# Kernel tuning notes

Hardware: AMD Instinct MI355X
Metric: run time of the kernel (lower is better)

Reference implementation:

```python
import jax, jax.numpy as jnp
import numpy as np

H, DH, M, ITERS, DIM = 8, 64, 256, 6, 512
SCALE = DH ** -0.5


def setup_inputs() -> dict:
    key = jax.random.key(0)
    ks = jax.random.split(key, 6)
    b, n, nz = 4, 8192, 4096  # multiples of M=256 -> padding branch is a no-op
    s = DIM ** -0.5
    x = jax.random.normal(ks[0], (b, n, DIM), jnp.float32)
    z = jax.random.normal(ks[1], (b, nz, DIM), jnp.float32)
    W_q = jax.random.normal(ks[2], (DIM, H * DH), jnp.float32) * s      # to_qkv[0] (no bias)
    W_kv = jax.random.normal(ks[3], (DIM, 2 * H * DH), jnp.float32) * s  # to_qkv[1] (no bias)
    W_out = jax.random.normal(ks[4], (H * DH, DIM), jnp.float32) * s     # to_out Linear
    b_out = jax.random.normal(ks[5], (DIM,), jnp.float32) * 0.01
    return {"x": x, "z": z, "W_q": W_q, "W_kv": W_kv, "W_out": W_out, "b_out": b_out}


def moore_penrose_pinv(a, iters=ITERS):
    # Newton-Schulz iterative pseudo-inverse (faithful to moore_penrose_iter_pinv)
    abs_a = jnp.abs(a)
    col = abs_a.sum(axis=-1)
    row = abs_a.sum(axis=-2)
    zt = jnp.swapaxes(a, -1, -2) / (jnp.max(col) * jnp.max(row))
    I = jnp.eye(a.shape[-1], dtype=a.dtype)
    for _ in range(iters):
        az = a @ zt
        zt = 0.25 * zt @ (13.0 * I - az @ (15.0 * I - az @ (7.0 * I - az)))
    return zt


def reference(x, z, W_q, W_kv, W_out, b_out):
    b, n, _ = x.shape
    nz = z.shape[1]
    l, lz = n // M, nz // M  # landmark group sizes (n, nz are multiples of M)

    # projections (dropout=0.1 is inactive at inference; self.norm is never applied in forward)
    q = (x @ W_q).reshape(b, n, H, DH).transpose(0, 2, 1, 3) * SCALE   # [b,h,n,dh]
    kv = z @ W_kv
    k = kv[..., : H * DH].reshape(b, nz, H, DH).transpose(0, 2, 1, 3)  # [b,h,nz,dh]
    v = kv[..., H * DH :].reshape(b, nz, H, DH).transpose(0, 2, 1, 3)  # [b,h,nz,dh]

    # landmarks: mean over groups of l (resp. lz) consecutive tokens
    q_land = q.reshape(b, H, M, l, DH).sum(axis=3) / l    # [b,h,M,dh]
    k_land = k.reshape(b, H, M, lz, DH).sum(axis=3) / lz  # [b,h,M,dh]

    sim1 = jnp.einsum('bhid,bhjd->bhij', q, k_land)       # [b,h,n,M]
    sim2 = jnp.einsum('bhid,bhjd->bhij', q_land, k_land)  # [b,h,M,M]
    sim3 = jnp.einsum('bhid,bhjd->bhij', q_land, k)       # [b,h,M,nz]
    attn1 = jax.nn.softmax(sim1, axis=-1)
    attn2 = jax.nn.softmax(sim2, axis=-1)
    attn3 = jax.nn.softmax(sim3, axis=-1)

    attn2_inv = moore_penrose_pinv(attn2)
    # (attn1 @ attn2_inv) @ (attn3 @ v) computed small-first for efficiency; same math
    out = attn1 @ (attn2_inv @ (attn3 @ v))               # [b,h,n,dh]  (residual=False)

    out = out.transpose(0, 2, 1, 3).reshape(b, n, H * DH)
    out = out @ W_out + b_out
    return x + out
```

## Files before the change

kernel.cpp:

```cpp
#include <hip/hip_runtime.h>

typedef unsigned short u16;
typedef __attribute__((ext_vector_type(8))) short bf16x8s;
typedef __attribute__((ext_vector_type(4))) float f32x4;

#define DEV static __device__ __forceinline__

DEV float b2f(u16 v) { return __uint_as_float(((unsigned)v) << 16); }
DEV u16 f2b(float f) {
  unsigned r;
  asm("v_cvt_pk_bf16_f32 %0, %1, %1" : "=v"(r) : "v"(f));
  return (u16)r;
}
DEV unsigned f2b2(float a, float b) {
  unsigned r;
  asm("v_cvt_pk_bf16_f32 %0, %1, %2" : "=v"(r) : "v"(a), "v"(b));
  return r;
}

#define GLL(gp, lp)                                                            \
  __builtin_amdgcn_global_load_lds(                                            \
      (const __attribute__((address_space(1))) unsigned int*)(gp),             \
      (__attribute__((address_space(3))) unsigned int*)(lp), 16, 0, 0)

#define MFMA __builtin_amdgcn_mfma_f32_16x16x32_bf16

__global__ __launch_bounds__(256) void k_f2bxz(const float* __restrict__ x,
                                               const float* __restrict__ z,
                                               u16* __restrict__ xb,
                                               u16* __restrict__ zb) {
  long i = (long)blockIdx.x * 256 + threadIdx.x;
  const float* src;
  u16* dst;
  long j;
  if (i < 4194304) { src = x; dst = xb; j = i; }
  else { src = z; dst = zb; j = i - 4194304; }
  float4 v = *(const float4*)(src + j * 4);
  unsigned* d = (unsigned*)(dst + j * 4);
  d[0] = f2b2(v.x, v.y);
  d[1] = f2b2(v.z, v.w);
}

__global__ __launch_bounds__(256) void k_wt3(const float* __restrict__ Wq,
                                             const float* __restrict__ Wkv,
                                             const float* __restrict__ Wo,
                                             u16* __restrict__ wqt,
                                             u16* __restrict__ wkvt,
                                             u16* __restrict__ wot) {
  int e = blockIdx.x * 256 + threadIdx.x;
  const float* W;
  u16* Wt;
  int N, le;
  if (e < 262144) { W = Wq; Wt = wqt; N = 512; le = e; }
  else if (e < 786432) { W = Wkv; Wt = wkvt; N = 1024; le = e - 262144; }
  else { W = Wo; Wt = wot; N = 512; le = e - 786432; }
  int nn = le >> 9, kk = le & 511;
  Wt[le] = f2b(W[(long)kk * N + nn]);
}

template <int MODE>
__global__ __launch_bounds__(256, 2) void k_gemm128(
    const u16* __restrict__ A, const u16* __restrict__ Bm, void* __restrict__ C0,
    void* __restrict__ C1, const float* __restrict__ xres,
    const float* __restrict__ bias, int K) {
  const int nwg = gridDim.x * gridDim.y;
  const int orig = blockIdx.y * gridDim.x + blockIdx.x;
  const int qq = nwg >> 3, rr = nwg & 7;
  const int xcd = orig & 7, loc = orig >> 3;
  const int swz = (xcd < rr ? xcd * (qq + 1) : rr * (qq + 1) + (xcd - rr) * qq) + loc;
  const int m0 = (swz / gridDim.x) << 7, n0 = (swz % gridDim.x) << 7;
  const int t = threadIdx.x, lane = t & 63, w = t >> 6;
  const int wm = (w >> 1) << 6, wn = (w & 1) << 6;
  const int fr = lane & 15, g = lane >> 4;
  __shared__ u16 As[8192];
  __shared__ u16 Bs[8192];
  f32x4 acc[4][4] = {};
  const int srow = t >> 3, scs = t & 7;
  for (int k0 = 0; k0 < K; k0 += 64) {
    __syncthreads();
#pragma unroll
    for (int i = 0; i < 4; ++i) {
      int row = srow + (i << 5), cs = scs;
      GLL(A + (long)(m0 + row) * K + k0 + ((cs ^ (row & 7)) << 3),
          &As[(i << 11) + (w << 9)]);
      GLL(Bm + (long)(n0 + row) * K + k0 + ((cs ^ (row & 7)) << 3),
          &Bs[(i << 11) + (w << 9)]);
    }
    __syncthreads();
#pragma unroll
    for (int ks = 0; ks < 2; ++ks) {
      bf16x8s af[4], bf[4];
#pragma unroll
      for (int fi = 0; fi < 4; ++fi) {
        int row = wm + fi * 16 + fr;
        af[fi] = *(const bf16x8s*)((const char*)As + row * 128 +
                                   (((ks * 4 + g) ^ (row & 7)) << 4));
      }
#pragma unroll
      for (int fj = 0; fj < 4; ++fj) {
        int row = wn + fj * 16 + fr;
        bf[fj] = *(const bf16x8s*)((const char*)Bs + row * 128 +
                                   (((ks * 4 + g) ^ (row & 7)) << 4));
      }
#pragma unroll
      for (int fi = 0; fi < 4; ++fi)
#pragma unroll
        for (int fj = 0; fj < 4; ++fj)
          acc[fi][fj] = MFMA(af[fi], bf[fj], acc[fi][fj], 0, 0, 0);
    }
  }
  const int crow = g << 2;
#pragma unroll
  for (int fi = 0; fi < 4; ++fi)
#pragma unroll
    for (int fj = 0; fj < 4; ++fj)
#pragma unroll
      for (int r = 0; r < 4; ++r) {
        int row = m0 + wm + fi * 16 + crow + r;
        int col = n0 + wn + fj * 16 + fr;
        float v = acc[fi][fj][r];
        if (MODE == 0) {
          int b = row >> 13, n = row & 8191, h = col >> 6, dh = col & 63;
          ((u16*)C0)[((((long)(b * 8 + h)) << 13) + n) * 64 + dh] = f2b(v * 0.125f);
        } else if (MODE == 1) {
          int b = row >> 12, nz = row & 4095;
          if (col < 512) {
            int h = col >> 6, dh = col & 63;
            ((u16*)C0)[((((long)(b * 8 + h)) << 12) + nz) * 64 + dh] = f2b(v);
          } else {
            int c2 = col - 512, h = c2 >> 6, dh = c2 & 63;
            ((u16*)C1)[((((long)(b * 8 + h) * 64 + dh)) << 12) + nz] = f2b(v);
          }
        } else if (MODE == 2) {
          long idx = ((long)row << 9) + col;
          ((float*)C0)[idx] = v + xres[idx] + bias[col];
        }
      }
}

__global__ __launch_bounds__(256) void k_land2(const u16* __restrict__ qb,
                                               const u16* __restrict__ kb,
                                               u16* __restrict__ qlh,
                                               u16* __restrict__ qll,
                                               u16* __restrict__ klh,
                                               u16* __restrict__ kll) {
  int pidx = blockIdx.x * 4 + (threadIdx.x >> 6);
  const u16* src;
  u16 *hi, *lo;
  int ntok, l;
  float inv;
  if (pidx < 8192) { src = qb; hi = qlh; lo = qll; ntok = 8192; l = 32; inv = 1.f / 32.f; }
  else { src = kb; hi = klh; lo = kll; ntok = 4096; l = 16; inv = 1.f / 16.f; pidx -= 8192; }
  int d = threadIdx.x & 63;
  int bh = pidx >> 8, m = pidx & 255;
  const u16* s = src + ((long)bh * ntok + (long)m * l) * 64 + d;
  float sum = 0.f;
  for (int j = 0; j < l; ++j) sum += b2f(s[j * 64]);
  sum *= inv;
  long o = ((long)bh * 256 + m) * 64 + d;
  u16 h = f2b(sum);
  hi[o] = h;
  lo[o] = f2b(sum - b2f(h));
}

__global__ __launch_bounds__(256, 2) void k_sim2(
    const u16* __restrict__ qlh, const u16* __restrict__ qll,
    const u16* __restrict__ klh, const u16* __restrict__ kll,
    float* __restrict__ attn2, u16* __restrict__ aNhi, u16* __restrict__ aNlo) {
  const int rb = blockIdx.x, bh = blockIdx.y;
  const int t = threadIdx.x, lane = t & 63, w = t >> 6;
  const int fr = lane & 15, g = lane >> 4;
  __shared__ char lds[65536];
  {
    const u16* kh = klh + (long)bh * 16384;
    const u16* kl = kll + (long)bh * 16384;
    int srow8 = lane >> 3, cs7 = lane & 7;
#pragma unroll
    for (int i = 0; i < 8; ++i) {
      int slab = w * 8 + i;
      int krow = slab * 8 + srow8;
      GLL(kh + krow * 64 + ((cs7 ^ (krow & 7)) << 3), lds + slab * 1024);
      GLL(kl + krow * 64 + ((cs7 ^ (krow & 7)) << 3), lds + 32768 + slab * 1024);
    }
  }
  long qoff = ((long)bh * 256 + rb * 64 + w * 16 + fr) * 64;
  bf16x8s qh0 = *(const bf16x8s*)(qlh + qoff + g * 8);
  bf16x8s qh1 = *(const bf16x8s*)(qlh + qoff + 32 + g * 8);
  bf16x8s ql0 = *(const bf16x8s*)(qll + qoff + g * 8);
  bf16x8s ql1 = *(const bf16x8s*)(qll + qoff + 32 + g * 8);
  __syncthreads();
  f32x4 s[16];
#pragma unroll
  for (int c = 0; c < 16; ++c) {
    int j = (c << 4) + fr;
    int o0 = j * 128 + ((g ^ (j & 7)) << 4);
    int o1 = j * 128 + (((4 + g) ^ (j & 7)) << 4);
    bf16x8s kh0 = *(const bf16x8s*)(lds + o0);
    bf16x8s kh1 = *(const bf16x8s*)(lds + o1);
    bf16x8s kl0 = *(const bf16x8s*)(lds + 32768 + o0);
    bf16x8s kl1 = *(const bf16x8s*)(lds + 32768 + o1);
    f32x4 zz = {};
    zz = MFMA(qh0, kh0, zz, 0, 0, 0);
    zz = MFMA(qh1, kh1, zz, 0, 0, 0);
    zz = MFMA(qh0, kl0, zz, 0, 0, 0);
    zz = MFMA(qh1, kl1, zz, 0, 0, 0);
    zz = MFMA(ql0, kh0, zz, 0, 0, 0);
    zz = MFMA(ql1, kh1, zz, 0, 0, 0);
    s[c] = zz;
  }
  float li[4];
#pragma unroll
  for (int r = 0; r < 4; ++r) {
    float m = s[0][r];
#pragma unroll
    for (int c = 1; c < 16; ++c) m = fmaxf(m, s[c][r]);
    m = fmaxf(m, __shfl_xor(m, 1, 64));
    m = fmaxf(m, __shfl_xor(m, 2, 64));
    m = fmaxf(m, __shfl_xor(m, 4, 64));
    m = fmaxf(m, __shfl_xor(m, 8, 64));
    float l = 0.f;
#pragma unroll
    for (int c = 0; c < 16; ++c) {
      float e = __expf(s[c][r] - m);
      s[c][r] = e;
      l += e;
    }
    l += __shfl_xor(l, 1, 64);
    l += __shfl_xor(l, 2, 64);
    l += __shfl_xor(l, 4, 64);
    l += __shfl_xor(l, 8, 64);
    li[r] = 1.f / l;
  }
#pragma unroll
  for (int c = 0; c < 16; ++c)
#pragma unroll
    for (int r = 0; r < 4; ++r) {
      int row = rb * 64 + w * 16 + (g << 2) + r;
      int col = (c << 4) + fr;
      long idx = ((long)bh << 16) + ((long)row << 8) + col;
      float p = s[c][r] * li[r];
      attn2[idx] = p;
      u16 h = f2b(p);
      aNhi[idx] = h;
      aNlo[idx] = f2b(p - b2f(h));
    }
}

__global__ __launch_bounds__(256) void k_colmax(const float* __restrict__ attn2,
                                                unsigned* __restrict__ cmax) {
  int bh = blockIdx.x, j = threadIdx.x, lane = j & 63, w = j >> 6;
  const float* p = attn2 + ((long)bh << 16) + j;
  float s = 0.f;
  for (int m = 0; m < 256; ++m) s += p[m * 256];
  float mx = s;
  for (int o = 1; o < 64; o <<= 1) mx = fmaxf(mx, __shfl_xor(mx, o, 64));
  __shared__ float r1[4];
  if (lane == 0) r1[w] = mx;
  __syncthreads();
  if (j == 0) {
    mx = fmaxf(fmaxf(r1[0], r1[1]), fmaxf(r1[2], r1[3]));
    atomicMax(cmax, __float_as_uint(mx));
  }
}

__global__ __launch_bounds__(256, 2) void k_t1part(
    const u16* __restrict__ qlb, const u16* __restrict__ kb,
    const u16* __restrict__ vtb, float* __restrict__ opart,
    float* __restrict__ pm_, float* __restrict__ pl_) {
  int orig = blockIdx.x;
  int xcd = orig & 7, idx = orig >> 3;
  int p = xcd * 16 + (idx >> 2);
  int rb = idx & 3;
  int bh = p >> 2, kc = p & 3;
  const int t = threadIdx.x, lane = t & 63, w = t >> 6;
  const int fr = lane & 15, g = lane >> 4;
  __shared__ char lds[65536];
  const u16* qrow = qlb + ((long)bh * 256 + rb * 64 + w * 16 + fr) * 64;
  bf16x8s qa0 = *(const bf16x8s*)(qrow + g * 8);
  bf16x8s qa1 = *(const bf16x8s*)(qrow + 32 + g * 8);
  f32x4 o[4] = {};
  float m[4] = {-3e38f, -3e38f, -3e38f, -3e38f};
  float l[4] = {};
  const long kbase = (long)bh * 262144;
  for (int cc = 0; cc < 4; ++cc) {
    int c0 = kc * 1024 + cc * 256;
    __syncthreads();
#pragma unroll
    for (int i = 0; i < 8; ++i) {
      int seg = (i << 8) + t, row = seg >> 3, cs = seg & 7;
      GLL(kb + kbase + (long)(c0 + row) * 64 + ((cs ^ (row & 7)) << 3),
          lds + (i << 12) + (w << 10));
    }
#pragma unroll
    for (int i = 0; i < 8; ++i) {
      int seg = (i << 8) + t, row = seg >> 5, cs = seg & 31;
      GLL(vtb + kbase + (long)row * 4096 + c0 + ((cs ^ (row & 7)) << 3),
          lds + 32768 + (i << 12) + (w << 10));
    }
    __syncthreads();
    f32x4 s[16];
#pragma unroll
    for (int c = 0; c < 16; ++c) {
      int j = c * 16 + fr;
      bf16x8s b0 = *(const bf16x8s*)(lds + j * 128 + ((g ^ (j & 7)) << 4));
      bf16x8s b1 = *(const bf16x8s*)(lds + j * 128 + (((4 + g) ^ (j & 7)) << 4));
      f32x4 zz = {};
      zz = MFMA(qa0, b0, zz, 0, 0, 0);
      zz = MFMA(qa1, b1, zz, 0, 0, 0);
      s[c] = zz;
    }
    float sc[4];
#pragma unroll
    for (int r = 0; r < 4; ++r) {
      float pm = s[0][r];
#pragma unroll
      for (int c = 1; c < 16; ++c) pm = fmaxf(pm, s[c][r]);
      pm = fmaxf(pm, __shfl_xor(pm, 1, 64));
      pm = fmaxf(pm, __shfl_xor(pm, 2, 64));
      pm = fmaxf(pm, __shfl_xor(pm, 4, 64));
      pm = fmaxf(pm, __shfl_xor(pm, 8, 64));
      float mn = fmaxf(m[r], pm);
      sc[r] = __expf(m[r] - mn);
      m[r] = mn;
    }
#pragma unroll
    for (int r = 0; r < 4; ++r) {
      float su = 0.f;
#pragma unroll
      for (int c = 0; c < 16; ++c) {
        float e = __expf(s[c][r] - m[r]);
        s[c][r] = e;
        su += e;
      }
      su += __shfl_xor(su, 1, 64);
      su += __shfl_xor(su, 2, 64);
      su += __shfl_xor(su, 4, 64);
      su += __shfl_xor(su, 8, 64);
      l[r] = l[r] * sc[r] + su;
    }
#pragma unroll
    for (int d = 0; d < 4; ++d)
#pragma unroll
      for (int r = 0; r < 4; ++r) o[d][r] *= sc[r];
    __syncthreads();
#pragma unroll
    for (int c = 0; c < 16; ++c)
#pragma unroll
      for (int r = 0; r < 4; ++r) {
        int row = (w << 4) + (g << 2) + r;
        int byin = (c << 5) + (fr << 1);
        *(u16*)(lds + row * 512 + (byin ^ ((row & 7) << 4))) = f2b(s[c][r]);
      }
    asm volatile("s_waitcnt lgkmcnt(0)" ::: "memory");
    __builtin_amdgcn_sched_barrier(0);
#pragma unroll
    for (int ss = 0; ss < 8; ++ss) {
      int prow = (w << 4) + fr;
      bf16x8s ap = *(const bf16x8s*)(lds + prow * 512 +
                                     (((ss * 64) + (g << 4)) ^ ((prow & 7) << 4)));
#pragma unroll
      for (int d = 0; d < 4; ++d) {
        int dh = (d << 4) + fr;
        bf16x8s bv = *(const bf16x8s*)(lds + 32768 + dh * 512 +
                                       (((ss * 4 + g) ^ (dh & 7)) << 4));
        o[d] = MFMA(ap, bv, o[d], 0, 0, 0);
      }
    }
  }
  __syncthreads();
  float* lf = (float*)lds;
#pragma unroll
  for (int d = 0; d < 4; ++d)
#pragma unroll
    for (int r = 0; r < 4; ++r)
      lf[((w << 4) + (g << 2) + r) * 76 + (d << 4) + fr] = o[d][r];
  __syncthreads();
  const long pb = (long)(bh * 4 + kc) * 256 + rb * 64;
#pragma unroll
  for (int i = 0; i < 4; ++i) {
    int row = i * 16 + (t >> 4);
    int c4 = (t & 15) << 2;
    float4 v = *(const float4*)&lf[row * 76 + c4];
    *(float4*)&opart[(pb + row) * 64 + c4] = v;
  }
  if (fr == 0) {
#pragma unroll
    for (int r = 0; r < 4; ++r) {
      int lr = (w << 4) + (g << 2) + r;
      pm_[pb + lr] = m[r];
      pl_[pb + lr] = l[r];
    }
  }
}

__global__ __launch_bounds__(256) void k_t1merge(
    const float* __restrict__ opart, const float* __restrict__ pm_,
    const float* __restrict__ pl_, u16* __restrict__ T1thi,
    u16* __restrict__ T1tlo) {
  const int rb = blockIdx.x, bh = blockIdx.y;
  const int t = threadIdx.x;
#pragma unroll
  for (int rp = 0; rp < 4; ++rp) {
    int row = rb * 64 + rp * 16 + (t >> 4);
    int dh4 = (t & 15) << 2;
    float pmv[4], M = -3e38f;
#pragma unroll
    for (int i = 0; i < 4; ++i) {
      pmv[i] = pm_[(long)(bh * 4 + i) * 256 + row];
      M = fmaxf(M, pmv[i]);
    }
    float L = 0.f, wt[4];
#pragma unroll
    for (int i = 0; i < 4; ++i) {
      wt[i] = __expf(pmv[i] - M);
      L += pl_[(long)(bh * 4 + i) * 256 + row] * wt[i];
    }
    float4 acc = {0.f, 0.f, 0.f, 0.f};
#pragma unroll
    for (int i = 0; i < 4; ++i) {
      float4 v = *(const float4*)&opart[((long)(bh * 4 + i) * 256 + row) * 64 + dh4];
      acc.x += v.x * wt[i]; acc.y += v.y * wt[i];
      acc.z += v.z * wt[i]; acc.w += v.w * wt[i];
    }
    float invL = 1.f / L;
    float vv[4] = {acc.x * invL, acc.y * invL, acc.z * invL, acc.w * invL};
#pragma unroll
    for (int e = 0; e < 4; ++e) {
      int dh = dh4 + e;
      long idx = (long)bh * 16384 + (long)dh * 256 + row;
      u16 h = f2b(vv[e]);
      T1thi[idx] = h;
      T1tlo[idx] = f2b(vv[e] - b2f(h));
    }
  }
}

template <int NP>
__global__ __launch_bounds__(256) void k_nn_mfma(
    const u16* __restrict__ Ahi, const u16* __restrict__ Alo,
    const u16* __restrict__ Bthi, const u16* __restrict__ Btlo,
    u16* __restrict__ CNhi, u16* __restrict__ CNlo,
    u16* __restrict__ CThi, u16* __restrict__ CTlo,
    int Nc, float sab, float sa, float cdiag) {
  const int bz = blockIdx.z;
  const long offA = (long)bz << 16;
  const long offB = (long)bz * ((long)Nc << 8);
  const int m0 = blockIdx.y << 6, n0 = blockIdx.x << 6;
  const int t = threadIdx.x, lane = t & 63, w = t >> 6;
  const int wm = (w >> 1) << 5, wn = (w & 1) << 5;
  const int fr = lane & 15, g = lane >> 4;
  __shared__ u16 lds[16384];
  u16* LAh = lds;
  u16* LAl = lds + 4096;
  u16* LBh = lds + 8192;
  u16* LBl = lds + 12288;
  f32x4 acc[2][2] = {};
  const int srow8 = lane >> 3, cs = lane & 7;
  for (int k0 = 0; k0 < 256; k0 += 64) {
    __syncthreads();
#pragma unroll
    for (int j = 0; j < 2; ++j) {
      int slab = w * 2 + j;
      int row = slab * 8 + srow8;
      long asrc = offA + (long)(m0 + row) * 256 + k0 + ((cs ^ (row & 7)) << 3);
      long bsrc = offB + (long)(n0 + row) * 256 + k0 + ((cs ^ (row & 7)) << 3);
      GLL(Ahi + asrc, LAh + slab * 512);
      GLL(Bthi + bsrc, LBh + slab * 512);
      if (NP == 3) {
        GLL(Alo + asrc, LAl + slab * 512);
        GLL(Btlo + bsrc, LBl + slab * 512);
      }
    }
    __syncthreads();
#pragma unroll
    for (int ks = 0; ks < 2; ++ks) {
      const int ra0 = wm + fr, ra1 = wm + 16 + fr;
      const int rb0 = wn + fr, rb1 = wn + 16 + fr;
#define RD(base, row) \
  (*(const bf16x8s*)((const char*)(base) + (row) * 128 + (((ks * 4 + g) ^ ((row) & 7)) << 4)))
      bf16x8s ah0 = RD(LAh, ra0), ah1 = RD(LAh, ra1);
      bf16x8s bh0 = RD(LBh, rb0), bh1 = RD(LBh, rb1);
      acc[0][0] = MFMA(ah0, bh0, acc[0][0], 0, 0, 0);
      acc[0][1] = MFMA(ah0, bh1, acc[0][1], 0, 0, 0);
      acc[1][0] = MFMA(ah1, bh0, acc[1][0], 0, 0, 0);
      acc[1][1] = MFMA(ah1, bh1, acc[1][1], 0, 0, 0);
      if (NP == 3) {
        bf16x8s al0 = RD(LAl, ra0), al1 = RD(LAl, ra1);
        bf16x8s bl0 = RD(LBl, rb0), bl1 = RD(LBl, rb1);
        acc[0][0] = MFMA(ah0, bl0, acc[0][0], 0, 0, 0);
        acc[0][0] = MFMA(al0, bh0, acc[0][0], 0, 0, 0);
        acc[0][1] = MFMA(ah0, bl1, acc[0][1], 0, 0, 0);
        acc[0][1] = MFMA(al0, bh1, acc[0][1], 0, 0, 0);
        acc[1][0] = MFMA(ah1, bl0, acc[1][0], 0, 0, 0);
        acc[1][0] = MFMA(al1, bh0, acc[1][0], 0, 0, 0);
        acc[1][1] = MFMA(ah1, bl1, acc[1][1], 0, 0, 0);
        acc[1][1] = MFMA(al1, bh1, acc[1][1], 0, 0, 0);
      }
#undef RD
    }
  }
  const int crow = g << 2;
  const long offC = (long)bz * ((long)Nc << 8);
#pragma unroll
  for (int i = 0; i < 2; ++i)
#pragma unroll
    for (int j = 0; j < 2; ++j)
#pragma unroll
      for (int r = 0; r < 4; ++r) {
        int row = m0 + wm + i * 16 + crow + r;
        int col = n0 + wn + j * 16 + fr;
        float v = sab * acc[i][j][r];
        if (sa != 0.f) {
          long ai = offA + ((long)row << 8) + col;
          v += sa * (b2f(Ahi[ai]) + b2f(Alo[ai]));
        }
        if (row == col) v += cdiag;
        if (CNhi) {
          long ci = offC + (long)row * Nc + col;
          u16 h = f2b(v);
          if (CNlo) { CNhi[ci] = h; CNlo[ci] = f2b(v - b2f(h)); }
          else CNhi[ci] = h;
        }
        if (CThi) {
          long ti = offC + ((long)col << 8) + row;
          u16 h = f2b(v);
          CThi[ti] = h;
          if (CTlo) CTlo[ti] = f2b(v - b2f(h));
        }
      }
}

__global__ __launch_bounds__(256) void k_prep_pinv(
    const float* __restrict__ attn2, const unsigned* __restrict__ cmax,
    u16* __restrict__ zNhi, u16* __restrict__ zNlo,
    u16* __restrict__ zThi, u16* __restrict__ zTlo) {
  const int bz = blockIdx.z, i0 = blockIdx.y << 6, j0 = blockIdx.x << 6;
  const float s = 1.f / __uint_as_float(*cmax);
  const float* base = attn2 + ((long)bz << 16);
  __shared__ float mt[64][65];
  const int r = threadIdx.x >> 2, cb = (threadIdx.x & 3) << 4;
#pragma unroll
  for (int c4 = 0; c4 < 16; c4 += 4) {
    float4 v = *(const float4*)&base[(long)(j0 + r) * 256 + i0 + cb + c4];
    mt[r][cb + c4] = v.x; mt[r][cb + c4 + 1] = v.y;
    mt[r][cb + c4 + 2] = v.z; mt[r][cb + c4 + 3] = v.w;
  }
  __syncthreads();
  const int i = i0 + r;
#pragma unroll
  for (int c4 = 0; c4 < 16; c4 += 4) {
    float4 v = *(const float4*)&base[(long)i * 256 + j0 + cb + c4];
    float vv[4] = {v.x, v.y, v.z, v.w};
#pragma unroll
    for (int e = 0; e < 4; ++e) {
      int j = j0 + cb + c4 + e;
      long idx = ((long)bz << 16) + ((long)i << 8) + j;
      float zt = vv[e] * s;
      u16 zh = f2b(zt);
      zThi[idx] = zh; zTlo[idx] = f2b(zt - b2f(zh));
      float zn = mt[cb + c4 + e][r] * s;
      u16 nh = f2b(zn);
      zNhi[idx] = nh; zNlo[idx] = f2b(zn - b2f(nh));
    }
  }
}

__global__ __launch_bounds__(256) void k_fused_attn1(const u16* __restrict__ q,
                                                     const u16* __restrict__ klb,
                                                     const u16* __restrict__ t2t,
                                                     u16* __restrict__ O) {
  const int bh = blockIdx.y, n0 = blockIdx.x << 6;
  const int bb = bh >> 3, hh = bh & 7;
  const int t = threadIdx.x, lane = t & 63, w = t >> 6;
  const int fr = lane & 15, g = lane >> 4;
  __shared__ char lds[65536];
  {
    const u16* ks = klb + (long)bh * 16384;
    const u16* ts = t2t + (long)bh * 16384;
    int srow8 = lane >> 3, cs7 = lane & 7;
    int srow2 = lane >> 5, seg32 = lane & 31;
#pragma unroll
    for (int i = 0; i < 8; ++i) {
      int slab = w * 8 + i;
      int krow = slab * 8 + srow8;
      GLL(ks + krow * 64 + ((cs7 ^ (krow & 7)) << 3), lds + slab * 1024);
      int trow = slab * 2 + srow2;
      GLL(ts + trow * 256 + ((seg32 ^ (trow & 7)) << 3), lds + 32768 + slab * 1024);
    }
  }
  __syncthreads();
  const u16* qrow = q + ((long)bh * 8192 + n0 + (w << 4) + fr) * 64;
  bf16x8s qa0 = *(const bf16x8s*)(qrow + g * 8);
  bf16x8s qa1 = *(const bf16x8s*)(qrow + 32 + g * 8);
  f32x4 s[16];
#pragma unroll
  for (int c = 0; c < 16; ++c) {
    int j = (c << 4) + fr;
    bf16x8s b0 = *(const bf16x8s*)(lds + j * 128 + ((g ^ (j & 7)) << 4));
    bf16x8s b1 = *(const bf16x8s*)(lds + j * 128 + (((4 + g) ^ (j & 7)) << 4));
    f32x4 zz = {};
    zz = MFMA(qa0, b0, zz, 0, 0, 0);
    zz = MFMA(qa1, b1, zz, 0, 0, 0);
    s[c] = zz;
  }
  float li[4];
#pragma unroll
  for (int r = 0; r < 4; ++r) {
    float m = s[0][r];
#pragma unroll
    for (int c = 1; c < 16; ++c) m = fmaxf(m, s[c][r]);
    m = fmaxf(m, __shfl_xor(m, 1, 64));
    m = fmaxf(m, __shfl_xor(m, 2, 64));
    m = fmaxf(m, __shfl_xor(m, 4, 64));
    m = fmaxf(m, __shfl_xor(m, 8, 64));
    float l = 0.f;
#pragma unroll
    for (int c = 0; c < 16; ++c) {
      float e = __expf(s[c][r] - m);
      s[c][r] = e;
      l += e;
    }
    l += __shfl_xor(l, 1, 64);
    l += __shfl_xor(l, 2, 64);
    l += __shfl_xor(l, 4, 64);
    l += __shfl_xor(l, 8, 64);
    li[r] = 1.f / l;
  }
  __syncthreads();
#pragma unroll
  for (int c = 0; c < 16; ++c)
#pragma unroll
    for (int r = 0; r < 4; ++r) {
      int row = (w << 4) + (g << 2) + r;
      int byin = (c << 5) + (fr << 1);
      *(u16*)(lds + row * 512 + (byin ^ ((row & 7) << 4))) = f2b(s[c][r]);
    }
  asm volatile("s_waitcnt lgkmcnt(0)" ::: "memory");
  __builtin_amdgcn_sched_barrier(0);
  f32x4 o4[4] = {};
#pragma unroll
  for (int ss = 0; ss < 8; ++ss) {
    int prow = (w << 4) + fr;
    bf16x8s ap = *(const bf16x8s*)(lds + prow * 512 +
                                   (((ss * 64) + (g << 4)) ^ ((prow & 7) << 4)));
#pragma unroll
    for (int d = 0; d < 4; ++d) {
      int dh = (d << 4) + fr;
      bf16x8s bv = *(const bf16x8s*)(lds + 32768 + dh * 512 +
                                     (((ss * 4 + g) ^ (dh & 7)) << 4));
      o4[d] = MFMA(ap, bv, o4[d], 0, 0, 0);
    }
  }
  u16* ob = O + (((long)bb * 8192 + n0 + (w << 4)) << 9) + (hh << 6);
#pragma unroll
  for (int d = 0; d < 4; ++d)
#pragma unroll
    for (int r = 0; r < 4; ++r) {
      int row = (g << 2) + r;
      int col = (d << 4) + fr;
      ob[((long)row << 9) + col] = f2b(o4[d][r] * li[r]);
    }
}

extern "C" void kernel_launch(void* const* d_in, const int* in_sizes, int n_in,
                              void* d_out, int out_size, void* d_ws, size_t ws_size,
                              hipStream_t stream) {
  const float* x = (const float*)d_in[0];
  const float* z = (const float*)d_in[1];
  const float* Wq = (const float*)d_in[2];
  const float* Wkv = (const float*)d_in[3];
  const float* Wo = (const float*)d_in[4];
  const float* bo = (const float*)d_in[5];
  float* out = (float*)d_out;

  char* base = (char*)d_ws;
  size_t off = 0;
  auto alloc = [&](size_t bytes) -> void* {
    void* r = base + off;
    off = (off + bytes + 255) & ~(size_t)255;
    return r;
  };
  u16* qb = (u16*)alloc(33554432);
  u16* kb = (u16*)alloc(16777216);
  u16* vtb = (u16*)alloc(16777216);
  u16* PS = (u16*)alloc(67108864);
  float* attn2 = (float*)alloc(8388608);
  u16* xb = (u16*)alloc(33554432);
  u16* zb = (u16*)alloc(16777216);
  u16* wqt = (u16*)alloc(524288);
  u16* wkvt = (u16*)alloc(1048576);
  u16* wot = (u16*)alloc(524288);
  u16* qlh = (u16*)alloc(1048576);
  u16* qll = (u16*)alloc(1048576);
  u16* klh = (u16*)alloc(1048576);
  u16* kll = (u16*)alloc(1048576);
  u16* T1t = (u16*)alloc(2097152);
  u16* T2t = (u16*)alloc(1048576);
  unsigned* cmax = (unsigned*)alloc(256);
  const long MC = 2097152;
  u16* P = PS;
  u16 *ztA_Nhi = P,          *ztA_Nlo = P + MC,      *ztA_Thi = P + 2 * MC,  *ztA_Tlo = P + 3 * MC;
  u16 *ztB_Nhi = P + 4 * MC,  *ztB_Nlo = P + 5 * MC,  *ztB_Thi = P + 6 * MC,  *ztB_Tlo = P + 7 * MC;
  u16 *az_Nhi = P + 8 * MC,   *az_Nlo = P + 9 * MC,   *az_Thi = P + 10 * MC,  *az_Tlo = P + 11 * MC;
  u16 *taThi = P + 12 * MC,   *taTlo = P + 13 * MC;
  u16 *tcThi = P + 14 * MC,   *tcTlo = P + 15 * MC;
  u16 *aNhi = zb, *aNlo = zb + MC;
  float* opart = (float*)PS;
  float* pm_ = opart + 2097152;
  float* pl_ = pm_ + 32768;
  u16* T1thi = T1t;
  u16* T1tlo = T1t + 524288;
  u16* Ob = xb;

  hipMemsetAsync(cmax, 0, 4, stream);
  k_f2bxz<<<24576, 256, 0, stream>>>(x, z, xb, zb);
  k_wt3<<<4096, 256, 0, stream>>>(Wq, Wkv, Wo, wqt, wkvt, wot);

  k_gemm128<0><<<dim3(4, 256), 256, 0, stream>>>(xb, wqt, qb, nullptr, nullptr,
                                                 nullptr, 512);
  k_gemm128<1><<<dim3(8, 128), 256, 0, stream>>>(zb, wkvt, kb, vtb, nullptr,
                                                 nullptr, 512);
  k_land2<<<4096, 256, 0, stream>>>(qb, kb, qlh, qll, klh, kll);

  k_sim2<<<dim3(4, 32), 256, 0, stream>>>(qlh, qll, klh, kll, attn2, aNhi, aNlo);
  k_colmax<<<32, 256, 0, stream>>>(attn2, cmax);

  k_t1part<<<512, 256, 0, stream>>>(qlh, kb, vtb, opart, pm_, pl_);
  k_t1merge<<<dim3(4, 32), 256, 0, stream>>>(opart, pm_, pl_, T1thi, T1tlo);

  k_prep_pinv<<<dim3(4, 4, 32), 256, 0, stream>>>(attn2, cmax, ztA_Nhi, ztA_Nlo,
                                                  ztA_Thi, ztA_Tlo);

  dim3 g256(4, 4, 32);
  u16 *cN0 = ztA_Nhi, *cN1 = ztA_Nlo, *cT0 = ztA_Thi, *cT1 = ztA_Tlo;
  u16 *nN0 = ztB_Nhi, *nN1 = ztB_Nlo, *nT0 = ztB_Thi, *nT1 = ztB_Tlo;
  for (int it = 0; it < 6; ++it) {
    bool last = (it == 5);
    if (it < 5) {
      k_nn_mfma<1><<<g256, 256, 0, stream>>>(aNhi, aNlo, cT0, cT1, az_Nhi, az_Nlo,
                                             az_Thi, az_Tlo, 256, 1.f, 0.f, 0.f);
      k_nn_mfma<1><<<g256, 256, 0, stream>>>(az_Nhi, az_Nlo, az_Thi, az_Tlo, nullptr,
                                             nullptr, taThi, taTlo, 256, 1.f, -7.f, 15.f);
      k_nn_mfma<1><<<g256, 256, 0, stream>>>(az_Nhi, az_Nlo, taThi, taTlo, nullptr,
                                             nullptr, tcThi, tcTlo, 256, -1.f, 0.f, 13.f);
      k_nn_mfma<1><<<g256, 256, 0, stream>>>(cN0, cN1, tcThi, tcTlo, nN0, nN1,
                                             nT0, nT1, 256, 0.25f, 0.f, 0.f);
    } else {
      k_nn_mfma<3><<<g256, 256, 0, stream>>>(aNhi, aNlo, cT0, cT1, az_Nhi, az_Nlo,
                                             az_Thi, az_Tlo, 256, 1.f, 0.f, 0.f);
      k_nn_mfma<3><<<g256, 256, 0, stream>>>(az_Nhi, az_Nlo, az_Thi, az_Tlo, nullptr,
                                             nullptr, taThi, taTlo, 256, 1.f, -7.f, 15.f);
      k_nn_mfma<3><<<g256, 256, 0, stream>>>(az_Nhi, az_Nlo, taThi, taTlo, nullptr,
                                             nullptr, tcThi, tcTlo, 256, -1.f, 0.f, 13.f);
      k_nn_mfma<3><<<g256, 256, 0, stream>>>(cN0, cN1, tcThi, tcTlo, nN0, nN1,
                                             last ? nullptr : nT0, last ? nullptr : nT1,
                                             256, 0.25f, 0.f, 0.f);
    }
    u16* t0;
    t0 = cN0; cN0 = nN0; nN0 = t0;  t0 = cN1; cN1 = nN1; nN1 = t0;
    t0 = cT0; cT0 = nT0; nT0 = t0;  t0 = cT1; cT1 = nT1; nT1 = t0;
  }
  k_nn_mfma<3><<<dim3(1, 4, 32), 256, 0, stream>>>(cN0, cN1, T1thi, T1tlo, nullptr,
                                                   nullptr, T2t, nullptr, 64,
                                                   1.f, 0.f, 0.f);

  k_fused_attn1<<<dim3(128, 32), 256, 0, stream>>>(qb, klh, T2t, Ob);
  k_gemm128<2><<<dim3(4, 256), 256, 0, stream>>>(Ob, wot, out, nullptr, x, bo, 512);
}
```

Before: 624.6 us.

## Fuse Newton-Schulz pseudo-inverse chain into one persistent per-head kernel

Replaces the 25 separate small-GEMM launches of the iterative pseudo-inverse, plus the final T2 product, with a single kernel. It runs one 512-thread block per batch-head, and each block computes full 256x256 products in sequence using 128KB of LDS. The aim is to remove kernel launch and inter-kernel drain overhead, and to stop writing some unused lo-precision transposed intermediates. In exchange only 32 workgroups run, so far fewer CUs are busy. Intermediates are still written to and re-read from global memory within one block, relying on __syncthreads for visibility, and loads are not overlapped with compute.

```diff
diff --git a/kernel.cpp b/kernel.cpp
--- a/kernel.cpp
+++ b/kernel.cpp
@@ -435,101 +435,6 @@
   }
 }
 
-template <int NP>
-__global__ __launch_bounds__(256) void k_nn_mfma(
-    const u16* __restrict__ Ahi, const u16* __restrict__ Alo,
-    const u16* __restrict__ Bthi, const u16* __restrict__ Btlo,
-    u16* __restrict__ CNhi, u16* __restrict__ CNlo,
-    u16* __restrict__ CThi, u16* __restrict__ CTlo,
-    int Nc, float sab, float sa, float cdiag) {
-  const int bz = blockIdx.z;
-  const long offA = (long)bz << 16;
-  const long offB = (long)bz * ((long)Nc << 8);
-  const int m0 = blockIdx.y << 6, n0 = blockIdx.x << 6;
-  const int t = threadIdx.x, lane = t & 63, w = t >> 6;
-  const int wm = (w >> 1) << 5, wn = (w & 1) << 5;
-  const int fr = lane & 15, g = lane >> 4;
-  __shared__ u16 lds[16384];
-  u16* LAh = lds;
-  u16* LAl = lds + 4096;
-  u16* LBh = lds + 8192;
-  u16* LBl = lds + 12288;
-  f32x4 acc[2][2] = {};
-  const int srow8 = lane >> 3, cs = lane & 7;
-  for (int k0 = 0; k0 < 256; k0 += 64) {
-    __syncthreads();
-#pragma unroll
-    for (int j = 0; j < 2; ++j) {
-      int slab = w * 2 + j;
-      int row = slab * 8 + srow8;
-      long asrc = offA + (long)(m0 + row) * 256 + k0 + ((cs ^ (row & 7)) << 3);
-      long bsrc = offB + (long)(n0 + row) * 256 + k0 + ((cs ^ (row & 7)) << 3);
-      GLL(Ahi + asrc, LAh + slab * 512);
-      GLL(Bthi + bsrc, LBh + slab * 512);
-      if (NP == 3) {
-        GLL(Alo + asrc, LAl + slab * 512);
-        GLL(Btlo + bsrc, LBl + slab * 512);
-      }
-    }
-    __syncthreads();
-#pragma unroll
-    for (int ks = 0; ks < 2; ++ks) {
-      const int ra0 = wm + fr, ra1 = wm + 16 + fr;
-      const int rb0 = wn + fr, rb1 = wn + 16 + fr;
-#define RD(base, row) \
-  (*(const bf16x8s*)((const char*)(base) + (row) * 128 + (((ks * 4 + g) ^ ((row) & 7)) << 4)))
-      bf16x8s ah0 = RD(LAh, ra0), ah1 = RD(LAh, ra1);
-      bf16x8s bh0 = RD(LBh, rb0), bh1 = RD(LBh, rb1);
-      acc[0][0] = MFMA(ah0, bh0, acc[0][0], 0, 0, 0);
-      acc[0][1] = MFMA(ah0, bh1, acc[0][1], 0, 0, 0);
-      acc[1][0] = MFMA(ah1, bh0, acc[1][0], 0, 0, 0);
-      acc[1][1] = MFMA(ah1, bh1, acc[1][1], 0, 0, 0);
-      if (NP == 3) {
-        bf16x8s al0 = RD(LAl, ra0), al1 = RD(LAl, ra1);
-        bf16x8s bl0 = RD(LBl, rb0), bl1 = RD(LBl, rb1);
-        acc[0][0] = MFMA(ah0, bl0, acc[0][0], 0, 0, 0);
-        acc[0][0] = MFMA(al0, bh0, acc[0][0], 0, 0, 0);
-        acc[0][1] = MFMA(ah0, bl1, acc[0][1], 0, 0, 0);
-        acc[0][1] = MFMA(al0, bh1, acc[0][1], 0, 0, 0);
-        acc[1][0] = MFMA(ah1, bl0, acc[1][0], 0, 0, 0);
-        acc[1][0] = MFMA(al1, bh0, acc[1][0], 0, 0, 0);
-        acc[1][1] = MFMA(ah1, bl1, acc[1][1], 0, 0, 0);
-        acc[1][1] = MFMA(al1, bh1, acc[1][1], 0, 0, 0);
-      }
-#undef RD
-    }
-  }
-  const int crow = g << 2;
-  const long offC = (long)bz * ((long)Nc << 8);
-#pragma unroll
-  for (int i = 0; i < 2; ++i)
-#pragma unroll
-    for (int j = 0; j < 2; ++j)
-#pragma unroll
-      for (int r = 0; r < 4; ++r) {
-        int row = m0 + wm + i * 16 + crow + r;
-        int col = n0 + wn + j * 16 + fr;
-        float v = sab * acc[i][j][r];
-        if (sa != 0.f) {
-          long ai = offA + ((long)row << 8) + col;
-          v += sa * (b2f(Ahi[ai]) + b2f(Alo[ai]));
-        }
-        if (row == col) v += cdiag;
-        if (CNhi) {
-          long ci = offC + (long)row * Nc + col;
-          u16 h = f2b(v);
-          if (CNlo) { CNhi[ci] = h; CNlo[ci] = f2b(v - b2f(h)); }
-          else CNhi[ci] = h;
-        }
-        if (CThi) {
-          long ti = offC + ((long)col << 8) + row;
-          u16 h = f2b(v);
-          CThi[ti] = h;
-          if (CTlo) CTlo[ti] = f2b(v - b2f(h));
-        }
-      }
-}
-
 __global__ __launch_bounds__(256) void k_prep_pinv(
     const float* __restrict__ attn2, const unsigned* __restrict__ cmax,
     u16* __restrict__ zNhi, u16* __restrict__ zNlo,
@@ -563,6 +468,138 @@
       zNhi[idx] = nh; zNlo[idx] = f2b(zn - b2f(nh));
     }
   }
+}
+
+template <int NP, int NC>
+DEV void chain_gemm(const u16* __restrict__ Ahi, const u16* __restrict__ Alo,
+                    const u16* __restrict__ Bthi, const u16* __restrict__ Btlo,
+                    u16* CNhi, u16* CNlo, u16* CThi, u16* CTlo,
+                    float sab, float sa, float cdiag, int bz, char* lds, int t) {
+  const int lane = t & 63, w = t >> 6;
+  const int fr = lane & 15, g = lane >> 4;
+  const long offA = (long)bz << 16;
+  const long offB = (long)bz * ((long)NC << 8);
+  const int wr = w << 5;
+  char* LA = lds;
+  char* LB = lds + 32768;
+  char* LAl = lds + 65536;
+  char* LBl = lds + 98304;
+  f32x4 acc[2][NC / 16] = {};
+  for (int k0 = 0; k0 < 256; k0 += 64) {
+    __syncthreads();
+#pragma unroll
+    for (int i = 0; i < 4; ++i) {
+      int seg = (i << 9) + t, row = seg >> 3, cs = seg & 7;
+      long a = offA + (long)row * 256 + k0 + ((cs ^ (row & 7)) << 3);
+      GLL(Ahi + a, LA + (i << 13) + (w << 10));
+      if (NP == 3) GLL(Alo + a, LAl + (i << 13) + (w << 10));
+    }
+#pragma unroll
+    for (int i = 0; i < NC / 64; ++i) {
+      int seg = (i << 9) + t, row = seg >> 3, cs = seg & 7;
+      long b = offB + (long)row * 256 + k0 + ((cs ^ (row & 7)) << 3);
+      GLL(Bthi + b, LB + (i << 13) + (w << 10));
+      if (NP == 3) GLL(Btlo + b, LBl + (i << 13) + (w << 10));
+    }
+    __syncthreads();
+#pragma unroll
+    for (int ks = 0; ks < 2; ++ks) {
+#define RD(base, row) \
+  (*(const bf16x8s*)((base) + (row) * 128 + (((ks * 4 + g) ^ ((row) & 7)) << 4)))
+      bf16x8s a0 = RD(LA, wr + fr), a1 = RD(LA, wr + 16 + fr);
+      bf16x8s l0, l1;
+      if (NP == 3) { l0 = RD(LAl, wr + fr); l1 = RD(LAl, wr + 16 + fr); }
+#pragma unroll
+      for (int c = 0; c < NC / 16; ++c) {
+        bf16x8s b0 = RD(LB, c * 16 + fr);
+        acc[0][c] = MFMA(a0, b0, acc[0][c], 0, 0, 0);
+        acc[1][c] = MFMA(a1, b0, acc[1][c], 0, 0, 0);
+        if (NP == 3) {
+          bf16x8s bl = RD(LBl, c * 16 + fr);
+          acc[0][c] = MFMA(a0, bl, acc[0][c], 0, 0, 0);
+          acc[0][c] = MFMA(l0, b0, acc[0][c], 0, 0, 0);
+          acc[1][c] = MFMA(a1, bl, acc[1][c], 0, 0, 0);
+          acc[1][c] = MFMA(l1, b0, acc[1][c], 0, 0, 0);
+        }
+      }
+#undef RD
+    }
+  }
+  const int crow = g << 2;
+  const long offC = (long)bz * ((long)NC << 8);
+#pragma unroll
+  for (int i = 0; i < 2; ++i)
+#pragma unroll
+    for (int c = 0; c < NC / 16; ++c)
+#pragma unroll
+      for (int r = 0; r < 4; ++r) {
+        int row = wr + i * 16 + crow + r;
+        int col = c * 16 + fr;
+        float v = sab * acc[i][c][r];
+        if (sa != 0.f) {
+          long ai = offA + ((long)row << 8) + col;
+          v += sa * (b2f(Ahi[ai]) + b2f(Alo[ai]));
+        }
+        if (row == col) v += cdiag;
+        if (CNhi) {
+          long ci = offC + (long)row * NC + col;
+          u16 h = f2b(v);
+          CNhi[ci] = h;
+          if (CNlo) CNlo[ci] = f2b(v - b2f(h));
+        }
+        if (CThi) {
+          long ti = offC + ((long)col << 8) + row;
+          u16 h = f2b(v);
+          CThi[ti] = h;
+          if (CTlo) CTlo[ti] = f2b(v - b2f(h));
+        }
+      }
+}
+
+__global__ __launch_bounds__(512) void k_pinv_chain(
+    const u16* __restrict__ aNhi, const u16* __restrict__ aNlo,
+    u16* __restrict__ PS, const u16* __restrict__ T1thi,
+    const u16* __restrict__ T1tlo, u16* __restrict__ T2t) {
+  __shared__ char lds[131072];
+  const int bz = blockIdx.x, t = threadIdx.x;
+  const long MC = 2097152;
+  u16 *zA_N0 = PS,          *zA_N1 = PS + MC,     *zA_T0 = PS + 2 * MC, *zA_T1 = PS + 3 * MC;
+  u16 *zB_N0 = PS + 4 * MC, *zB_N1 = PS + 5 * MC, *zB_T0 = PS + 6 * MC, *zB_T1 = PS + 7 * MC;
+  u16 *azN0 = PS + 8 * MC,  *azN1 = PS + 9 * MC,  *azT0 = PS + 10 * MC, *azT1 = PS + 11 * MC;
+  u16 *taT0 = PS + 12 * MC, *taT1 = PS + 13 * MC;
+  u16 *tcT0 = PS + 14 * MC, *tcT1 = PS + 15 * MC;
+  for (int it = 0; it < 6; ++it) {
+    u16 *cN0, *cN1, *cT0, *cT1, *nN0, *nN1, *nT0, *nT1;
+    if ((it & 1) == 0) {
+      cN0 = zA_N0; cN1 = zA_N1; cT0 = zA_T0; cT1 = zA_T1;
+      nN0 = zB_N0; nN1 = zB_N1; nT0 = zB_T0; nT1 = zB_T1;
+    } else {
+      cN0 = zB_N0; cN1 = zB_N1; cT0 = zB_T0; cT1 = zB_T1;
+      nN0 = zA_N0; nN1 = zA_N1; nT0 = zA_T0; nT1 = zA_T1;
+    }
+    if (it < 5) {
+      bool l4 = (it == 4);
+      chain_gemm<1, 256>(aNhi, aNlo, cT0, cT1, azN0, azN1, azT0, nullptr,
+                         1.f, 0.f, 0.f, bz, lds, t);
+      chain_gemm<1, 256>(azN0, azN1, azT0, nullptr, nullptr, nullptr, taT0, nullptr,
+                         1.f, -7.f, 15.f, bz, lds, t);
+      chain_gemm<1, 256>(azN0, azN1, taT0, nullptr, nullptr, nullptr, tcT0, nullptr,
+                         -1.f, 0.f, 13.f, bz, lds, t);
+      chain_gemm<1, 256>(cN0, cN1, tcT0, nullptr, nN0, l4 ? nN1 : nullptr,
+                         nT0, l4 ? nT1 : nullptr, 0.25f, 0.f, 0.f, bz, lds, t);
+    } else {
+      chain_gemm<3, 256>(aNhi, aNlo, cT0, cT1, azN0, azN1, azT0, azT1,
+                         1.f, 0.f, 0.f, bz, lds, t);
+      chain_gemm<3, 256>(azN0, azN1, azT0, azT1, nullptr, nullptr, taT0, taT1,
+                         1.f, -7.f, 15.f, bz, lds, t);
+      chain_gemm<3, 256>(azN0, azN1, taT0, taT1, nullptr, nullptr, tcT0, tcT1,
+                         -1.f, 0.f, 13.f, bz, lds, t);
+      chain_gemm<3, 256>(cN0, cN1, tcT0, tcT1, nN0, nN1, nullptr, nullptr,
+                         0.25f, 0.f, 0.f, bz, lds, t);
+    }
+  }
+  chain_gemm<3, 64>(zA_N0, zA_N1, T1thi, T1tlo, nullptr, nullptr, T2t, nullptr,
+                    1.f, 0.f, 0.f, bz, lds, t);
 }
 
 __global__ __launch_bounds__(256) void k_fused_attn1(const u16* __restrict__ q,
@@ -698,12 +735,7 @@
   u16* T2t = (u16*)alloc(1048576);
   unsigned* cmax = (unsigned*)alloc(256);
   const long MC = 2097152;
-  u16* P = PS;
-  u16 *ztA_Nhi = P,          *ztA_Nlo = P + MC,      *ztA_Thi = P + 2 * MC,  *ztA_Tlo = P + 3 * MC;
-  u16 *ztB_Nhi = P + 4 * MC,  *ztB_Nlo = P + 5 * MC,  *ztB_Thi = P + 6 * MC,  *ztB_Tlo = P + 7 * MC;
-  u16 *az_Nhi = P + 8 * MC,   *az_Nlo = P + 9 * MC,   *az_Thi = P + 10 * MC,  *az_Tlo = P + 11 * MC;
-  u16 *taThi = P + 12 * MC,   *taTlo = P + 13 * MC;
-  u16 *tcThi = P + 14 * MC,   *tcTlo = P + 15 * MC;
+  u16 *ztA_Nhi = PS, *ztA_Nlo = PS + MC, *ztA_Thi = PS + 2 * MC, *ztA_Tlo = PS + 3 * MC;
   u16 *aNhi = zb, *aNlo = zb + MC;
   float* opart = (float*)PS;
   float* pm_ = opart + 2097152;
@@ -730,39 +762,7 @@
 
   k_prep_pinv<<<dim3(4, 4, 32), 256, 0, stream>>>(attn2, cmax, ztA_Nhi, ztA_Nlo,
                                                   ztA_Thi, ztA_Tlo);
-
-  dim3 g256(4, 4, 32);
-  u16 *cN0 = ztA_Nhi, *cN1 = ztA_Nlo, *cT0 = ztA_Thi, *cT1 = ztA_Tlo;
-  u16 *nN0 = ztB_Nhi, *nN1 = ztB_Nlo, *nT0 = ztB_Thi, *nT1 = ztB_Tlo;
-  for (int it = 0; it < 6; ++it) {
-    bool last = (it == 5);
-    if (it < 5) {
-      k_nn_mfma<1><<<g256, 256, 0, stream>>>(aNhi, aNlo, cT0, cT1, az_Nhi, az_Nlo,
-                                             az_Thi, az_Tlo, 256, 1.f, 0.f, 0.f);
-      k_nn_mfma<1><<<g256, 256, 0, stream>>>(az_Nhi, az_Nlo, az_Thi, az_Tlo, nullptr,
-                                             nullptr, taThi, taTlo, 256, 1.f, -7.f, 15.f);
-      k_nn_mfma<1><<<g256, 256, 0, stream>>>(az_Nhi, az_Nlo, taThi, taTlo, nullptr,
-                                             nullptr, tcThi, tcTlo, 256, -1.f, 0.f, 13.f);
-      k_nn_mfma<1><<<g256, 256, 0, stream>>>(cN0, cN1, tcThi, tcTlo, nN0, nN1,
-                                             nT0, nT1, 256, 0.25f, 0.f, 0.f);
-    } else {
-      k_nn_mfma<3><<<g256, 256, 0, stream>>>(aNhi, aNlo, cT0, cT1, az_Nhi, az_Nlo,
-                                             az_Thi, az_Tlo, 256, 1.f, 0.f, 0.f);
-      k_nn_mfma<3><<<g256, 256, 0, stream>>>(az_Nhi, az_Nlo, az_Thi, az_Tlo, nullptr,
-                                             nullptr, taThi, taTlo, 256, 1.f, -7.f, 15.f);
-      k_nn_mfma<3><<<g256, 256, 0, stream>>>(az_Nhi, az_Nlo, taThi, taTlo, nullptr,
-                                             nullptr, tcThi, tcTlo, 256, -1.f, 0.f, 13.f);
-      k_nn_mfma<3><<<g256, 256, 0, stream>>>(cN0, cN1, tcThi, tcTlo, nN0, nN1,
-                                             last ? nullptr : nT0, last ? nullptr : nT1,
-                                             256, 0.25f, 0.f, 0.f);
-    }
-    u16* t0;
-    t0 = cN0; cN0 = nN0; nN0 = t0;  t0 = cN1; cN1 = nN1; nN1 = t0;
-    t0 = cT0; cT0 = nT0; nT0 = t0;  t0 = cT1; cT1 = nT1; nT1 = t0;
-  }
-  k_nn_mfma<3><<<dim3(1, 4, 32), 256, 0, stream>>>(cN0, cN1, T1thi, T1tlo, nullptr,
-                                                   nullptr, T2t, nullptr, 64,
-                                                   1.f, 0.f, 0.f);
+  k_pinv_chain<<<32, 512, 0, stream>>>(aNhi, aNlo, PS, T1thi, T1tlo, T2t);
 
   k_fused_attn1<<<dim3(128, 32), 256, 0, stream>>>(qb, klh, T2t, Ob);
   k_gemm128<2><<<dim3(4, 256), 256, 0, stream>>>(Ob, wot, out, nullptr, x, bo, 512);
```

After: 2.468 ms. +295.1%, slower.
